# Kernel tuning notes

Hardware: AMD Instinct MI355X
Metric: run time of the kernel (lower is better)

## Reference

```python
import jax, jax.numpy as jnp
import numpy as np

B, N, H, D, C = 2, 4096, 16, 64, 1024  # batch, tokens, heads, head_dim, codebook_size


def setup_inputs() -> dict:
    key = jax.random.key(0)
    k0, k1, k2, k3 = jax.random.split(key, 4)
    x = jax.random.normal(k0, (B, N, H * D), dtype=jnp.float32)
    codebooks = jax.random.normal(k1, (H, C, D), dtype=jnp.float32)  # nn.Parameter(randn)
    # EinMix 'h n d -> h n c' weights, shape (h, d, c), uniform-ish init scaled by 1/sqrt(d)
    wk = jax.random.normal(k2, (H, D, D), dtype=jnp.float32) / np.sqrt(D)
    wv = jax.random.normal(k3, (H, D, D), dtype=jnp.float32) / np.sqrt(D)
    return {"x": x, "codebooks": codebooks, "wk": wk, "wv": wv}


def reference(x, codebooks, wk, wv):
    # Eval-mode forward of Memcodes (argmax + one-hot selection).
    b, n, feat = x.shape
    h, c, d = codebooks.shape
    scale = d ** -0.5
    # b n (h d) -> b h n d, scaled
    q = x.reshape(b, n, h, d).transpose(0, 2, 1, 3) * scale
    # per-head linear projections of the codebooks (EinMix: h n d -> h n c)
    k = jnp.einsum('hnd,hdc->hnc', codebooks, wk)
    v = jnp.einsum('hnd,hdc->hnc', codebooks, wv)
    # attention-style logits against codebook keys: b h i j
    logits = jnp.einsum('bhid,hjd->bhij', q, k)
    codebook_indices = jnp.argmax(logits, axis=-1)          # b h i
    attn = jax.nn.one_hot(codebook_indices, c, dtype=logits.dtype)  # b h i j
    # one-hot matmul gather of values (as in the original module)
    out = jnp.einsum('bhij,hjd->bhid', attn, v)
    out = out.transpose(0, 2, 1, 3).reshape(b, n, h * d)    # b n (h d)
    # perplexity per head
    mean = attn.mean(axis=(0, 2))                           # h s
    perp = jnp.exp(-jnp.sum(mean * jnp.log(mean + 1e-10), axis=-1))  # h
    return out, codebook_indices, perp
```

## Files before the change

### kernel.cpp

```cpp
#include <hip/hip_runtime.h>
#include <cstdint>
#include <cfloat>

#define B_ 2
#define N_ 4096
#define H_ 16
#define D_ 64
#define C_ 1024

#define TI 128
#define CJ 64
#define QP 72
#define EPS 4e-3f

typedef unsigned short u16;
typedef unsigned int   u32;
typedef __attribute__((ext_vector_type(8))) short short8;
typedef __attribute__((ext_vector_type(4))) float f32x4;

__device__ __forceinline__ float bf2f(u16 s) {
    u32 u = ((u32)s) << 16;
    return __uint_as_float(u);
}
__device__ __forceinline__ u16 f2bf(float f) {
    u32 u = __float_as_uint(f);
    return (u16)((u + 0x7fffu + ((u >> 16) & 1u)) >> 16);
}
__device__ __forceinline__ void cf(float& a, float& b) {
    float t = fmaxf(a, b);
    b = fminf(a, b);
    a = t;
}

__global__ __launch_bounds__(256, 2)
void proj_kernel(const float* __restrict__ cb,
                 const float* __restrict__ wk,
                 const float* __restrict__ wv,
                 float* __restrict__ k32,
                 float* __restrict__ v32,
                 u16* __restrict__ khi,
                 u16* __restrict__ klo,
                 u32* __restrict__ ghist) {
    int h  = blockIdx.x >> 5;
    int jc = blockIdx.x & 31;
    int tid = threadIdx.x;
    int wid  = tid >> 6;
    int lane = tid & 63;

    if (jc == 0) {
        ghist[h * C_ + tid]       = 0u;
        ghist[h * C_ + tid + 256] = 0u;
        ghist[h * C_ + tid + 512] = 0u;
        ghist[h * C_ + tid + 768] = 0u;
    }

    const float* wkh = wk + (size_t)h * D_ * D_ + lane;
    const float* wvh = wv + (size_t)h * D_ * D_ + lane;
    float wkc[D_], wvc[D_];
#pragma unroll
    for (int d = 0; d < D_; ++d) {
        wkc[d] = wkh[(size_t)d * D_];
        wvc[d] = wvh[(size_t)d * D_];
    }

#pragma unroll 1
    for (int i = 0; i < 8; ++i) {
        int jl  = wid * 8 + i;
        int row = jc * 32 + jl;
        float cv = cb[((size_t)h * C_ + row) * D_ + lane];
        float ak = 0.f, av = 0.f;
#pragma unroll
        for (int d = 0; d < D_; ++d) {
            float s = __int_as_float(__builtin_amdgcn_readlane(__float_as_int(cv), d));
            ak = fmaf(s, wkc[d], ak);
            av = fmaf(s, wvc[d], av);
        }
        size_t o = ((size_t)h * C_ + row) * D_ + lane;
        k32[o] = ak;
        v32[o] = av;
        u16 hi = f2bf(ak);
        khi[o] = hi;
        klo[o] = f2bf(ak - bf2f(hi));
    }
}

__global__ __launch_bounds__(256, 4)
void tile_kernel(const float* __restrict__ x,
                 const u16* __restrict__ khi,
                 const u16* __restrict__ klo,
                 const float* __restrict__ k32,
                 const float* __restrict__ v32,
                 u32* __restrict__ ghist,
                 float* __restrict__ out,
                 float* __restrict__ idx_out) {
    __shared__ __align__(16) u16 smem[TI * QP * 2];
    u16* qhi_s = smem;
    u16* qlo_s = smem + TI * QP;
    const int HBUF = CJ * QP;

    int blk = blockIdx.x;
    int it = blk & 31;
    int bh = blk >> 5;
    int h = bh & (H_ - 1);
    int b = bh >> 4;
    int i0 = it * TI;
    int tid = threadIdx.x;
    int w    = tid >> 6;
    int lane = tid & 63;
    int lm   = lane & 15;
    int lq   = lane >> 4;
    int rowbase = (b * H_ + h) * N_ + i0;

    {
        const float* xb = x + ((size_t)(b * N_ + i0) * (H_ * D_)) + h * D_;
#pragma unroll
        for (int i = 0; i < 8; ++i) {
            int e4  = tid + 256 * i;
            int row = e4 >> 4;
            int c4  = (e4 & 15) * 4;
            float4 v = *(const float4*)(xb + (size_t)row * (H_ * D_) + c4);
            v.x *= 0.125f; v.y *= 0.125f; v.z *= 0.125f; v.w *= 0.125f;
            u16 h0 = f2bf(v.x), h1 = f2bf(v.y), h2 = f2bf(v.z), h3 = f2bf(v.w);
            u16 l0 = f2bf(v.x - bf2f(h0)), l1 = f2bf(v.y - bf2f(h1));
            u16 l2 = f2bf(v.z - bf2f(h2)), l3 = f2bf(v.w - bf2f(h3));
            uint2 ph = make_uint2((u32)h0 | ((u32)h1 << 16), (u32)h2 | ((u32)h3 << 16));
            uint2 pl = make_uint2((u32)l0 | ((u32)l1 << 16), (u32)l2 | ((u32)l3 << 16));
            *(uint2*)&qhi_s[row * QP + c4] = ph;
            *(uint2*)&qlo_s[row * QP + c4] = pl;
        }
    }
    __syncthreads();

    short8 ahi[2][2], alo[2][2];
#pragma unroll
    for (int g = 0; g < 2; ++g) {
        int base = (w * 32 + g * 16 + lm) * QP;
        ahi[g][0] = *(const short8*)&qhi_s[base + lq * 8];
        ahi[g][1] = *(const short8*)&qhi_s[base + 32 + lq * 8];
        alo[g][0] = *(const short8*)&qlo_s[base + lq * 8];
        alo[g][1] = *(const short8*)&qlo_s[base + 32 + lq * 8];
    }
    __syncthreads();

    float b1[2][4], b2[2][4];
#pragma unroll
    for (int g = 0; g < 2; ++g)
#pragma unroll
        for (int r = 0; r < 4; ++r) { b1[g][r] = -FLT_MAX; b2[g][r] = -FLT_MAX; }

    const u16* khg = khi + (size_t)h * C_ * D_;
    const u16* klg = klo + (size_t)h * C_ * D_;

    int srow = tid >> 3;
    int sc8  = (tid & 7) * 8;

    {
        const uint4* gh = (const uint4*)khg;
        const uint4* gl = (const uint4*)klg;
        uint4 a0 = gh[tid], a1 = gh[tid + 256];
        uint4 c0 = gl[tid], c1 = gl[tid + 256];
        *(uint4*)&smem[srow * QP + sc8]               = a0;
        *(uint4*)&smem[(srow + 32) * QP + sc8]        = a1;
        *(uint4*)&smem[HBUF + srow * QP + sc8]        = c0;
        *(uint4*)&smem[HBUF + (srow + 32) * QP + sc8] = c1;
    }
    __syncthreads();

#pragma unroll 1
    for (int ch = 0; ch < C_ / CJ; ++ch) {
        uint4 p0, p1, p2, p3;
        bool pf = (ch + 1 < C_ / CJ);
        if (pf) {
            const uint4* gh = (const uint4*)(khg + (size_t)(ch + 1) * CJ * D_);
            const uint4* gl = (const uint4*)(klg + (size_t)(ch + 1) * CJ * D_);
            p0 = gh[tid]; p1 = gh[tid + 256];
            p2 = gl[tid]; p3 = gl[tid + 256];
        }

        const u16* khc = smem + (ch & 1) * 2 * HBUF;
        const u16* klc = khc + HBUF;
        int jb = ch * CJ;

#pragma unroll
        for (int t = 0; t < 4; ++t) {
            const u16* bhp = &khc[(t * 16 + lm) * QP + lq * 8];
            const u16* blp = &klc[(t * 16 + lm) * QP + lq * 8];
            short8 bh0 = *(const short8*)bhp;
            short8 bh1 = *(const short8*)(bhp + 32);
            short8 bl0 = *(const short8*)blp;
            short8 bl1 = *(const short8*)(blp + 32);
            int rj = 1023 - (jb + t * 16 + lm);

#pragma unroll
            for (int g = 0; g < 2; ++g) {
                f32x4 acc = {0.f, 0.f, 0.f, 0.f};
                acc = __builtin_amdgcn_mfma_f32_16x16x32_bf16(ahi[g][0], bh0, acc, 0, 0, 0);
                acc = __builtin_amdgcn_mfma_f32_16x16x32_bf16(ahi[g][1], bh1, acc, 0, 0, 0);
                acc = __builtin_amdgcn_mfma_f32_16x16x32_bf16(ahi[g][0], bl0, acc, 0, 0, 0);
                acc = __builtin_amdgcn_mfma_f32_16x16x32_bf16(ahi[g][1], bl1, acc, 0, 0, 0);
                acc = __builtin_amdgcn_mfma_f32_16x16x32_bf16(alo[g][0], bh0, acc, 0, 0, 0);
                acc = __builtin_amdgcn_mfma_f32_16x16x32_bf16(alo[g][1], bh1, acc, 0, 0, 0);
#pragma unroll
                for (int r = 0; r < 4; ++r) {
                    int pb = (__float_as_int(acc[r]) & 0xFFFFFC00) | rj;
                    float pv = __int_as_float(pb);
                    b2[g][r] = __builtin_amdgcn_fmed3f(pv, b1[g][r], b2[g][r]);
                    b1[g][r] = fmaxf(pv, b1[g][r]);
                }
            }
        }

        if (pf) {
            u16* wh = smem + ((ch + 1) & 1) * 2 * HBUF;
            u16* wl = wh + HBUF;
            *(uint4*)&wh[srow * QP + sc8]        = p0;
            *(uint4*)&wh[(srow + 32) * QP + sc8] = p1;
            *(uint4*)&wl[srow * QP + sc8]        = p2;
            *(uint4*)&wl[(srow + 32) * QP + sc8] = p3;
            __syncthreads();
        }
    }

    float m0[2][4], m1[2][4], m2[2][4], m3[2][4];
#pragma unroll
    for (int g = 0; g < 2; ++g)
#pragma unroll
    for (int r = 0; r < 4; ++r) {
        float e0 = b1[g][r], e1 = b2[g][r], e2 = -FLT_MAX, e3 = -FLT_MAX;
#pragma unroll
        for (int off = 1; off < 16; off <<= 1) {
            float e7 = __shfl_xor(e0, off, 16);
            float e6 = __shfl_xor(e1, off, 16);
            float e5 = __shfl_xor(e2, off, 16);
            float e4 = __shfl_xor(e3, off, 16);
            cf(e0, e4); cf(e1, e5); cf(e2, e6); cf(e3, e7);
            cf(e0, e2); cf(e1, e3); cf(e0, e1); cf(e2, e3);
        }
        m0[g][r] = e0; m1[g][r] = e1; m2[g][r] = e2; m3[g][r] = e3;
    }

    const float* vh = v32 + (size_t)h * C_ * D_;
    float* ob = out + ((size_t)(b * N_ + i0) * (H_ * D_)) + h * D_;

#define DOT(jj, dst)                                                          \
        {                                                                     \
            float kv = k32[((size_t)h * C_ + (jj)) * D_ + lane];              \
            float a2 = 0.f;                                                   \
            _Pragma("unroll")                                                 \
            for (int c = 3; c >= 0; --c) {                                    \
                float qq = __shfl(qv, (lane & 15) + c * 16, 64);              \
                float kk = __shfl(kv, (lane & 15) + c * 16, 64);              \
                a2 = fmaf(qq, kk, a2);                                        \
            }                                                                 \
            _Pragma("unroll")                                                 \
            for (int off2 = 8; off2 >= 1; off2 >>= 1)                         \
                a2 += __shfl_xor(a2, off2, 16);                               \
            dst = a2;                                                         \
        }

#pragma unroll
    for (int g = 0; g < 2; ++g)
#pragma unroll
    for (int r = 0; r < 4; ++r) {
#pragma unroll 1
        for (int q = 0; q < 4; ++q) {
            int rl = w * 32 + g * 16 + q * 4 + r;
            int src = q * 16;
            float e0 = __shfl(m0[g][r], src, 64);
            float e1 = __shfl(m1[g][r], src, 64);
            float e2 = __shfl(m2[g][r], src, 64);
            float e3 = __shfl(m3[g][r], src, 64);

            int nc = 1;
            if (e0 - e1 < EPS) {
                nc = 2;
                if (e0 - e2 < EPS) {
                    nc = 3;
                    if (e0 - e3 < EPS) nc = 4;
                }
            }

            int j0 = (1023 - (__float_as_int(e0) & 1023)) & (C_ - 1);
            int bj = j0;
            float outv = (float)bj;

            if (nc > 1) {
                int j1 = (1023 - (__float_as_int(e1) & 1023)) & (C_ - 1);
                int j2 = (1023 - (__float_as_int(e2) & 1023)) & (C_ - 1);
                int j3 = (1023 - (__float_as_int(e3) & 1023)) & (C_ - 1);
                float qv = x[((size_t)(b * N_ + i0 + rl)) * (H_ * D_) + h * D_ + lane] * 0.125f;
                float sc0, sc1, sc2, sc3;
                DOT(j0, sc0)
                DOT(j1, sc1)
                sc2 = -FLT_MAX; sc3 = -FLT_MAX;
                if (nc > 2) DOT(j2, sc2)
                if (nc > 3) DOT(j3, sc3)

                float bs = sc0;
                float ss = -FLT_MAX; int sj = bj;
                {
                    float s = sc1; int j = j1;
                    if (s > bs || (s == bs && j < bj)) { ss = bs; sj = bj; bs = s; bj = j; }
                    else if (s > ss || (s == ss && j < sj)) { ss = s; sj = j; }
                }
                if (nc > 2) {
                    float s = sc2; int j = j2;
                    if (s > bs || (s == bs && j < bj)) { ss = bs; sj = bj; bs = s; bj = j; }
                    else if (s > ss || (s == ss && j < sj)) { ss = s; sj = j; }
                }
                if (nc > 3) {
                    float s = sc3; int j = j3;
                    if (s > bs || (s == bs && j < bj)) { ss = bs; sj = bj; bs = s; bj = j; }
                    else if (s > ss || (s == ss && j < sj)) { ss = s; sj = j; }
                }
                outv = (float)bj;
                int dj = bj > sj ? bj - sj : sj - bj;
                if (bs - ss < 1e-6f && dj <= 36 && dj > 0) outv = 0.5f * (float)(bj + sj);
            }

            if (lane == 0) {
                idx_out[(size_t)rowbase + rl] = outv;
                atomicAdd(&ghist[h * C_ + (((int)(outv + 0.25f)) & (C_ - 1))], 1u);
            }
            ob[(size_t)rl * (H_ * D_) + lane] = vh[(size_t)bj * D_ + lane];
        }
    }
#undef DOT
}

__global__ __launch_bounds__(256)
void perp_kernel(const u32* __restrict__ ghist, float* __restrict__ perp_out) {
    __shared__ float red[256];
    int h = blockIdx.x;
    int tid = threadIdx.x;

    float s = 0.f;
    for (int i = tid; i < C_; i += 256) {
        float p = (float)ghist[h * C_ + i] * (1.0f / (B_ * N_));
        s += p * logf(p + 1e-10f);
    }
    red[tid] = s;
    __syncthreads();
    for (int st = 128; st > 0; st >>= 1) {
        if (tid < st) red[tid] += red[tid + st];
        __syncthreads();
    }
    if (tid == 0) perp_out[h] = expf(-red[0]);
}

extern "C" void kernel_launch(void* const* d_in, const int* in_sizes, int n_in,
                              void* d_out, int out_size, void* d_ws, size_t ws_size,
                              hipStream_t stream) {
    (void)in_sizes; (void)n_in; (void)out_size; (void)ws_size;
    const float* x  = (const float*)d_in[0];
    const float* cb = (const float*)d_in[1];
    const float* wk = (const float*)d_in[2];
    const float* wv = (const float*)d_in[3];

    float* out      = (float*)d_out;
    float* idx_out  = out + (size_t)B_ * N_ * H_ * D_;
    float* perp_out = idx_out + (size_t)B_ * H_ * N_;

    float* k32   = (float*)d_ws;
    float* v32   = k32 + (size_t)H_ * C_ * D_;
    u16*   khi   = (u16*)(v32 + (size_t)H_ * C_ * D_);
    u16*   klo   = khi + (size_t)H_ * C_ * D_;
    u32*   ghist = (u32*)(klo + (size_t)H_ * C_ * D_);

    proj_kernel<<<H_ * 32, 256, 0, stream>>>(cb, wk, wv, k32, v32, khi, klo, ghist);
    tile_kernel<<<B_ * H_ * (N_ / TI), 256, 0, stream>>>(x, khi, klo, k32, v32, ghist,
                                                         out, idx_out);
    perp_kernel<<<H_, 256, 0, stream>>>(ghist, perp_out);
}
```

Measured before the change: 165.8 us.

## Load Q fragments directly from global, halve codebook chunk, raise occupancy

```diff
diff --git a/kernel.cpp b/kernel.cpp
--- a/kernel.cpp
+++ b/kernel.cpp
@@ -9,7 +9,7 @@
 #define C_ 1024
 
 #define TI 128
-#define CJ 64
+#define CJ 32
 #define QP 72
 #define EPS 4e-3f
 
@@ -30,6 +30,20 @@
     float t = fmaxf(a, b);
     b = fminf(a, b);
     a = t;
+}
+__device__ __forceinline__ void split8(float4 a, float4 b, short8& hi, short8& lo) {
+    float v0 = a.x * 0.125f, v1 = a.y * 0.125f, v2 = a.z * 0.125f, v3 = a.w * 0.125f;
+    float v4 = b.x * 0.125f, v5 = b.y * 0.125f, v6 = b.z * 0.125f, v7 = b.w * 0.125f;
+    u16 h0 = f2bf(v0), h1 = f2bf(v1), h2 = f2bf(v2), h3 = f2bf(v3);
+    u16 h4 = f2bf(v4), h5 = f2bf(v5), h6 = f2bf(v6), h7 = f2bf(v7);
+    short8 h8, l8;
+    h8[0] = (short)h0; h8[1] = (short)h1; h8[2] = (short)h2; h8[3] = (short)h3;
+    h8[4] = (short)h4; h8[5] = (short)h5; h8[6] = (short)h6; h8[7] = (short)h7;
+    l8[0] = (short)f2bf(v0 - bf2f(h0)); l8[1] = (short)f2bf(v1 - bf2f(h1));
+    l8[2] = (short)f2bf(v2 - bf2f(h2)); l8[3] = (short)f2bf(v3 - bf2f(h3));
+    l8[4] = (short)f2bf(v4 - bf2f(h4)); l8[5] = (short)f2bf(v5 - bf2f(h5));
+    l8[6] = (short)f2bf(v6 - bf2f(h6)); l8[7] = (short)f2bf(v7 - bf2f(h7));
+    hi = h8; lo = l8;
 }
 
 __global__ __launch_bounds__(256, 2)
@@ -84,7 +98,7 @@
     }
 }
 
-__global__ __launch_bounds__(256, 4)
+__global__ __launch_bounds__(256, 8)
 void tile_kernel(const float* __restrict__ x,
                  const u16* __restrict__ khi,
                  const u16* __restrict__ klo,
@@ -93,9 +107,7 @@
                  u32* __restrict__ ghist,
                  float* __restrict__ out,
                  float* __restrict__ idx_out) {
-    __shared__ __align__(16) u16 smem[TI * QP * 2];
-    u16* qhi_s = smem;
-    u16* qlo_s = smem + TI * QP;
+    __shared__ __align__(16) u16 smem[4 * CJ * QP];
     const int HBUF = CJ * QP;
 
     int blk = blockIdx.x;
@@ -111,70 +123,52 @@
     int lq   = lane >> 4;
     int rowbase = (b * H_ + h) * N_ + i0;
 
-    {
-        const float* xb = x + ((size_t)(b * N_ + i0) * (H_ * D_)) + h * D_;
-#pragma unroll
-        for (int i = 0; i < 8; ++i) {
-            int e4  = tid + 256 * i;
-            int row = e4 >> 4;
-            int c4  = (e4 & 15) * 4;
-            float4 v = *(const float4*)(xb + (size_t)row * (H_ * D_) + c4);
-            v.x *= 0.125f; v.y *= 0.125f; v.z *= 0.125f; v.w *= 0.125f;
-            u16 h0 = f2bf(v.x), h1 = f2bf(v.y), h2 = f2bf(v.z), h3 = f2bf(v.w);
-            u16 l0 = f2bf(v.x - bf2f(h0)), l1 = f2bf(v.y - bf2f(h1));
-            u16 l2 = f2bf(v.z - bf2f(h2)), l3 = f2bf(v.w - bf2f(h3));
-            uint2 ph = make_uint2((u32)h0 | ((u32)h1 << 16), (u32)h2 | ((u32)h3 << 16));
-            uint2 pl = make_uint2((u32)l0 | ((u32)l1 << 16), (u32)l2 | ((u32)l3 << 16));
-            *(uint2*)&qhi_s[row * QP + c4] = ph;
-            *(uint2*)&qlo_s[row * QP + c4] = pl;
-        }
-    }
-    __syncthreads();
-
-    short8 ahi[2][2], alo[2][2];
-#pragma unroll
-    for (int g = 0; g < 2; ++g) {
-        int base = (w * 32 + g * 16 + lm) * QP;
-        ahi[g][0] = *(const short8*)&qhi_s[base + lq * 8];
-        ahi[g][1] = *(const short8*)&qhi_s[base + 32 + lq * 8];
-        alo[g][0] = *(const short8*)&qlo_s[base + lq * 8];
-        alo[g][1] = *(const short8*)&qlo_s[base + 32 + lq * 8];
-    }
-    __syncthreads();
-
-    float b1[2][4], b2[2][4];
-#pragma unroll
-    for (int g = 0; g < 2; ++g)
-#pragma unroll
-        for (int r = 0; r < 4; ++r) { b1[g][r] = -FLT_MAX; b2[g][r] = -FLT_MAX; }
-
     const u16* khg = khi + (size_t)h * C_ * D_;
     const u16* klg = klo + (size_t)h * C_ * D_;
 
     int srow = tid >> 3;
     int sc8  = (tid & 7) * 8;
 
+    uint4 a0, c0;
     {
         const uint4* gh = (const uint4*)khg;
         const uint4* gl = (const uint4*)klg;
-        uint4 a0 = gh[tid], a1 = gh[tid + 256];
-        uint4 c0 = gl[tid], c1 = gl[tid + 256];
-        *(uint4*)&smem[srow * QP + sc8]               = a0;
-        *(uint4*)&smem[(srow + 32) * QP + sc8]        = a1;
-        *(uint4*)&smem[HBUF + srow * QP + sc8]        = c0;
-        *(uint4*)&smem[HBUF + (srow + 32) * QP + sc8] = c1;
-    }
+        a0 = gh[tid];
+        c0 = gl[tid];
+    }
+
+    short8 ahi[2][2], alo[2][2];
+#pragma unroll
+    for (int g = 0; g < 2; ++g) {
+        int row = i0 + w * 32 + g * 16 + lm;
+        const float* xr = x + ((size_t)(b * N_ + row)) * (H_ * D_) + h * D_ + lq * 8;
+        float4 q0 = *(const float4*)(xr);
+        float4 q1 = *(const float4*)(xr + 4);
+        float4 q2 = *(const float4*)(xr + 32);
+        float4 q3 = *(const float4*)(xr + 36);
+        split8(q0, q1, ahi[g][0], alo[g][0]);
+        split8(q2, q3, ahi[g][1], alo[g][1]);
+    }
+
+    float b1[2][4], b2[2][4];
+#pragma unroll
+    for (int g = 0; g < 2; ++g)
+#pragma unroll
+        for (int r = 0; r < 4; ++r) { b1[g][r] = -FLT_MAX; b2[g][r] = -FLT_MAX; }
+
+    *(uint4*)&smem[srow * QP + sc8]        = a0;
+    *(uint4*)&smem[HBUF + srow * QP + sc8] = c0;
     __syncthreads();
 
 #pragma unroll 1
     for (int ch = 0; ch < C_ / CJ; ++ch) {
-        uint4 p0, p1, p2, p3;
+        uint4 p0, p2;
         bool pf = (ch + 1 < C_ / CJ);
         if (pf) {
             const uint4* gh = (const uint4*)(khg + (size_t)(ch + 1) * CJ * D_);
             const uint4* gl = (const uint4*)(klg + (size_t)(ch + 1) * CJ * D_);
-            p0 = gh[tid]; p1 = gh[tid + 256];
-            p2 = gl[tid]; p3 = gl[tid + 256];
+            p0 = gh[tid];
+            p2 = gl[tid];
         }
 
         const u16* khc = smem + (ch & 1) * 2 * HBUF;
@@ -182,7 +176,7 @@
         int jb = ch * CJ;
 
 #pragma unroll
-        for (int t = 0; t < 4; ++t) {
+        for (int t = 0; t < 2; ++t) {
             const u16* bhp = &khc[(t * 16 + lm) * QP + lq * 8];
             const u16* blp = &klc[(t * 16 + lm) * QP + lq * 8];
             short8 bh0 = *(const short8*)bhp;
@@ -213,10 +207,8 @@
         if (pf) {
             u16* wh = smem + ((ch + 1) & 1) * 2 * HBUF;
             u16* wl = wh + HBUF;
-            *(uint4*)&wh[srow * QP + sc8]        = p0;
-            *(uint4*)&wh[(srow + 32) * QP + sc8] = p1;
-            *(uint4*)&wl[srow * QP + sc8]        = p2;
-            *(uint4*)&wl[(srow + 32) * QP + sc8] = p3;
+            *(uint4*)&wh[srow * QP + sc8] = p0;
+            *(uint4*)&wl[srow * QP + sc8] = p2;
             __syncthreads();
         }
     }
```

After: 479.3 us. +189.0%, slower.
